# Performance work log

Hardware: AMD Instinct MI355X
Metric: run time of the kernel (lower is better)

Reference implementation:

```python
import jax, jax.numpy as jnp
import numpy as np
import math

B, S, HID = 2, 2048, 2048
NH, NKV, HD = 32, 8, 64
THETA = 10000.0
EPS = 1e-6
LAYER_IDX = 1
LAMBDA_INIT = 0.8 - 0.6 * math.exp(-0.3 * LAYER_IDX)
LAMBDA_STD = 0.1


def setup_inputs() -> dict:
    key = jax.random.key(0)
    ks = jax.random.split(key, 10)
    hidden_states = jax.random.normal(ks[0], (B, S, HID), jnp.float32)
    # RoPE cos/sin, llama convention: emb = cat(freqs, freqs)
    inv_freq = 1.0 / (THETA ** (np.arange(0, HD, 2, dtype=np.float32) / HD))
    freqs = np.outer(np.arange(S, dtype=np.float32), inv_freq)  # [S, HD/2]
    emb = np.concatenate([freqs, freqs], axis=-1)                # [S, HD]
    cos = jnp.broadcast_to(jnp.asarray(np.cos(emb), jnp.float32)[None], (B, S, HD))
    sin = jnp.broadcast_to(jnp.asarray(np.sin(emb), jnp.float32)[None], (B, S, HD))
    # additive causal mask [B,1,S,S]
    causal = jnp.triu(jnp.full((S, S), -1e9, dtype=jnp.float32), k=1)
    attention_mask = jnp.broadcast_to(causal[None, None], (B, 1, S, S))
    sc = 0.02
    wq = sc * jax.random.normal(ks[1], (NH * HD, HID), jnp.float32)
    wk = sc * jax.random.normal(ks[2], (NKV * HD, HID), jnp.float32)
    wv = sc * jax.random.normal(ks[3], (NKV * HD, HID), jnp.float32)
    wo = sc * jax.random.normal(ks[4], (HID, NH * HD), jnp.float32)
    lambda_q1 = LAMBDA_STD * jax.random.normal(ks[5], (HD,), jnp.float32)
    lambda_k1 = LAMBDA_STD * jax.random.normal(ks[6], (HD,), jnp.float32)
    lambda_q2 = LAMBDA_STD * jax.random.normal(ks[7], (HD,), jnp.float32)
    lambda_k2 = LAMBDA_STD * jax.random.normal(ks[8], (HD,), jnp.float32)
    return {"hidden_states": hidden_states, "cos": cos, "sin": sin,
            "attention_mask": attention_mask, "wq": wq, "wk": wk, "wv": wv,
            "wo": wo, "lambda_q1": lambda_q1, "lambda_k1": lambda_k1,
            "lambda_q2": lambda_q2, "lambda_k2": lambda_k2}


def _rotate_half(x):
    x1, x2 = jnp.split(x, 2, axis=-1)
    return jnp.concatenate([-x2, x1], axis=-1)


def reference(hidden_states, cos, sin, attention_mask, wq, wk, wv, wo,
              lambda_q1, lambda_k1, lambda_q2, lambda_k2):
    b, s, _ = hidden_states.shape
    # projections -> [b, h, s, d]
    q = jnp.einsum('bsh,oh->bso', hidden_states, wq).reshape(b, s, NH, HD).transpose(0, 2, 1, 3)
    k = jnp.einsum('bsh,oh->bso', hidden_states, wk).reshape(b, s, NKV, HD).transpose(0, 2, 1, 3)
    v = jnp.einsum('bsh,oh->bso', hidden_states, wv).reshape(b, s, NKV, HD).transpose(0, 2, 1, 3)
    # rotary
    c, sn = cos[:, None], sin[:, None]  # [b,1,s,d]
    q = q * c + _rotate_half(q) * sn
    k = k * c + _rotate_half(k) * sn
    # GQA repeat
    groups = NH // NKV
    k = jnp.repeat(k, groups, axis=1)
    v = jnp.repeat(v, groups, axis=1)
    # diff-attention value trick: pair head i with head i+NH/2 -> [b, NH, s, 2d]
    v = jnp.concatenate([v[:, :NH // 2], v[:, NH // 2:]], axis=-1)  # [b, NH/2, s, 2d]
    v = jnp.concatenate([v, v], axis=1)                              # [b, NH, s, 2d]
    # scores + causal mask, stable softmax in fp32
    aw = jnp.einsum('bhqd,bhkd->bhqk', q, k) / math.sqrt(HD)
    aw = aw + attention_mask
    aw = jax.nn.softmax(aw.astype(jnp.float32), axis=-1).astype(q.dtype)
    ao = jnp.einsum('bhqk,bhkd->bhqd', aw, v)  # [b, NH, s, 2d]
    lam1 = jnp.exp(jnp.sum((lambda_q1 * lambda_k1).astype(jnp.float32)))
    lam2 = jnp.exp(jnp.sum((lambda_q2 * lambda_k2).astype(jnp.float32)))
    lam = (lam1 - lam2).astype(q.dtype) + LAMBDA_INIT
    a1, a2 = ao[:, :NH // 2], ao[:, NH // 2:]
    out = a1 - lam * a2  # [b, NH/2, s, 2d]
    # RMSNorm over last dim (no affine)
    out = out * jax.lax.rsqrt(jnp.mean(out * out, axis=-1, keepdims=True) + EPS)
    out = (1.0 - LAMBDA_INIT) * out
    out = out.transpose(0, 2, 1, 3).reshape(b, s, NH * HD)
    return jnp.einsum('bso,ho->bsh', out, wo)
```

## Files before the change

### kernel.cpp

```cpp
#include <hip/hip_runtime.h>

typedef __attribute__((ext_vector_type(8))) short bhalf8;
typedef __attribute__((ext_vector_type(4))) float floatx4;

constexpr int B_ = 2, S_ = 2048, HID_ = 2048, NH_ = 32, NKV_ = 8, HD_ = 64;
constexpr float LAMBDA_INIT_F = 0.35550906759096924f;
constexpr float EPS_ = 1e-6f;
constexpr float QSCALE_ = 0.18033688011112042f;

#define DEVINL __device__ __forceinline__

DEVINL float bf2f(unsigned short u) {
    union { unsigned u; float f; } v; v.u = ((unsigned)u) << 16; return v.f;
}
DEVINL unsigned short f2bf(float f) {
    union { float f; unsigned u; } v; v.f = f;
    unsigned u = v.u;
    return (unsigned short)((u + 0x7fffu + ((u >> 16) & 1u)) >> 16);
}
DEVINL float fexp2(float x) {
#if __has_builtin(__builtin_amdgcn_exp2f)
    return __builtin_amdgcn_exp2f(x);
#else
    return exp2f(x);
#endif
}
DEVINL unsigned pk_bf16(float a, float b) {
#if __has_builtin(__builtin_amdgcn_cvt_pk_bf16_f32)
    typedef __bf16 bf16x2_t __attribute__((ext_vector_type(2)));
    bf16x2_t p = __builtin_amdgcn_cvt_pk_bf16_f32(a, b);
    unsigned r;
    __builtin_memcpy(&r, &p, 4);
    return r;
#else
    return (unsigned)f2bf(a) | ((unsigned)f2bf(b) << 16);
#endif
}
DEVINL void load_lds16(const unsigned short* g, unsigned short* l) {
    __builtin_amdgcn_global_load_lds(
        (const __attribute__((address_space(1))) unsigned int*)g,
        (__attribute__((address_space(3))) unsigned int*)l, 16, 0, 0);
}

__global__ void cvt_f32_bf16(const float* __restrict__ src, unsigned short* __restrict__ dst, int n) {
    int i = (blockIdx.x * 256 + threadIdx.x) * 4;
    if (i < n) {
        float4 v = *(const float4*)(src + i);
        ushort4 o;
        o.x = f2bf(v.x); o.y = f2bf(v.y); o.z = f2bf(v.z); o.w = f2bf(v.w);
        *(ushort4*)(dst + i) = o;
    }
}

__global__ void lam_kernel(const float* __restrict__ q1, const float* __restrict__ k1,
                           const float* __restrict__ q2, const float* __restrict__ k2,
                           float* __restrict__ lam) {
    const int l = threadIdx.x;
    float p1 = q1[l] * k1[l];
    float p2 = q2[l] * k2[l];
    #pragma unroll
    for (int off = 1; off < 64; off <<= 1) {
        p1 += __shfl_xor(p1, off, 64);
        p2 += __shfl_xor(p2, off, 64);
    }
    if (l == 0) *lam = expf(p1) - expf(p2) + LAMBDA_INIT_F;
}

template <bool OUT_BF16>
__global__ __launch_bounds__(256)
void gemm_bt(const unsigned short* __restrict__ A, const unsigned short* __restrict__ Bw,
             void* __restrict__ Cout, int M, int N, int K) {
    __shared__ __align__(16) unsigned short As[2][128][32];
    __shared__ __align__(16) unsigned short Bs[2][128][32];
    const int t = threadIdx.x;
    const int w = t >> 6, lane = t & 63, quad = lane >> 4, lid = lane & 15;
    const int wr = (w >> 1) * 64, wc = (w & 1) * 64;
    const long bm = (long)blockIdx.x * 128, bn = (long)blockIdx.y * 128;

    floatx4 acc[4][4];
    #pragma unroll
    for (int i = 0; i < 4; i++)
        #pragma unroll
        for (int j = 0; j < 4; j++) acc[i][j] = (floatx4){0.f, 0.f, 0.f, 0.f};

    const int s0 = t, s1 = t + 256;
    const unsigned short* Ag0 = A + (bm + (s0 >> 2)) * (long)K + (s0 & 3) * 8;
    const unsigned short* Ag1 = A + (bm + (s1 >> 2)) * (long)K + (s1 & 3) * 8;
    const unsigned short* Bg0 = Bw + (bn + (s0 >> 2)) * (long)K + (s0 & 3) * 8;
    const unsigned short* Bg1 = Bw + (bn + (s1 >> 2)) * (long)K + (s1 & 3) * 8;
    const int l0 = s0 * 8, l1 = s1 * 8;

    load_lds16(Ag0, &As[0][0][0] + l0);
    load_lds16(Ag1, &As[0][0][0] + l1);
    load_lds16(Bg0, &Bs[0][0][0] + l0);
    load_lds16(Bg1, &Bs[0][0][0] + l1);
    __syncthreads();

    const int nk = K >> 5;
    for (int kt = 0; kt < nk; kt++) {
        const int cur = kt & 1, nxt = cur ^ 1;
        if (kt + 1 < nk) {
            const int off = (kt + 1) << 5;
            load_lds16(Ag0 + off, &As[nxt][0][0] + l0);
            load_lds16(Ag1 + off, &As[nxt][0][0] + l1);
            load_lds16(Bg0 + off, &Bs[nxt][0][0] + l0);
            load_lds16(Bg1 + off, &Bs[nxt][0][0] + l1);
        }
        bhalf8 af[4], bf[4];
        #pragma unroll
        for (int i = 0; i < 4; i++) af[i] = *(const bhalf8*)&As[cur][wr + i * 16 + lid][quad * 8];
        #pragma unroll
        for (int j = 0; j < 4; j++) bf[j] = *(const bhalf8*)&Bs[cur][wc + j * 16 + lid][quad * 8];
        #pragma unroll
        for (int i = 0; i < 4; i++)
            #pragma unroll
            for (int j = 0; j < 4; j++)
                acc[i][j] = __builtin_amdgcn_mfma_f32_16x16x32_bf16(af[i], bf[j], acc[i][j], 0, 0, 0);
        __syncthreads();
    }

    #pragma unroll
    for (int i = 0; i < 4; i++) {
        #pragma unroll
        for (int j = 0; j < 4; j++) {
            const long row = bm + wr + i * 16 + quad * 4;
            const long col = bn + wc + j * 16 + lid;
            #pragma unroll
            for (int r = 0; r < 4; r++) {
                float v = acc[i][j][r];
                if (OUT_BF16)
                    ((unsigned short*)Cout)[(row + r) * N + col] = f2bf(v);
                else
                    ((float*)Cout)[(row + r) * N + col] = v;
            }
        }
    }
}

__global__ __launch_bounds__(256)
void rope_split(const unsigned short* __restrict__ qkv, const float* __restrict__ cosb,
                const float* __restrict__ sinb, unsigned short* __restrict__ Qr,
                unsigned short* __restrict__ Kr) {
    const int r = blockIdx.x;
    const int b = r >> 11, s = r & 2047;
    const int t = threadIdx.x;
    const unsigned short* rowp = qkv + (size_t)r * 3072;
    const float* cp = cosb + (size_t)r * 64;
    const float* sp = sinb + (size_t)r * 64;
    {
        const int h = t >> 3, d0 = (t & 7) * 8;
        unsigned short x[8], o[8], y[8];
        *(int4*)x = *(const int4*)(rowp + h * 64 + d0);
        const int od = (d0 < 32) ? d0 + 32 : d0 - 32;
        *(int4*)o = *(const int4*)(rowp + h * 64 + od);
        const float sgn = (d0 < 32) ? -1.f : 1.f;
        float cc[8], sn[8];
        *(float4*)&cc[0] = *(const float4*)(cp + d0);
        *(float4*)&cc[4] = *(const float4*)(cp + d0 + 4);
        *(float4*)&sn[0] = *(const float4*)(sp + d0);
        *(float4*)&sn[4] = *(const float4*)(sp + d0 + 4);
        #pragma unroll
        for (int i = 0; i < 8; i++)
            y[i] = f2bf((bf2f(x[i]) * cc[i] + sgn * bf2f(o[i]) * sn[i]) * QSCALE_);
        *(int4*)(Qr + ((size_t)(b * NH_ + h) * S_ + s) * HD_ + d0) = *(const int4*)y;
    }
    if (t < 64) {
        const int h = t >> 3, d0 = (t & 7) * 8;
        unsigned short x[8], o[8], y[8];
        *(int4*)x = *(const int4*)(rowp + 2048 + h * 64 + d0);
        const int od = (d0 < 32) ? d0 + 32 : d0 - 32;
        *(int4*)o = *(const int4*)(rowp + 2048 + h * 64 + od);
        const float sgn = (d0 < 32) ? -1.f : 1.f;
        float cc[8], sn[8];
        *(float4*)&cc[0] = *(const float4*)(cp + d0);
        *(float4*)&cc[4] = *(const float4*)(cp + d0 + 4);
        *(float4*)&sn[0] = *(const float4*)(sp + d0);
        *(float4*)&sn[4] = *(const float4*)(sp + d0 + 4);
        #pragma unroll
        for (int i = 0; i < 8; i++)
            y[i] = f2bf(bf2f(x[i]) * cc[i] + sgn * bf2f(o[i]) * sn[i]);
        *(int4*)(Kr + ((size_t)(b * NKV_ + h) * S_ + s) * HD_ + d0) = *(const int4*)y;
    }
}

__global__ __launch_bounds__(256)
void transpose_v(const unsigned short* __restrict__ qkv, unsigned short* __restrict__ VT) {
    __shared__ __align__(16) unsigned short tile[64][72];
    const int bh = blockIdx.y;
    const int b = bh >> 3, h = bh & 7;
    const int s0 = blockIdx.x * 64;
    const int t = threadIdx.x;
    {
        const int sl = t >> 2, d0 = (t & 3) * 16;
        const unsigned short* src = qkv + (size_t)(b * 2048 + s0 + sl) * 3072 + 2560 + h * 64 + d0;
        *(int4*)&tile[sl][d0] = *(const int4*)src;
        *(int4*)&tile[sl][d0 + 8] = *(const int4*)(src + 8);
    }
    __syncthreads();
    {
        const int dl = t >> 2, sc0 = (t & 3) * 16;
        unsigned short* dst = VT + ((size_t)bh * 64 + dl) * 2048 + s0 + sc0;
        unsigned short out[16];
        #pragma unroll
        for (int i = 0; i < 16; i++) out[i] = tile[sc0 + i][dl];
        *(int4*)dst = *(const int4*)&out[0];
        *(int4*)(dst + 8) = *(const int4*)&out[8];
    }
}

__global__ __launch_bounds__(512, 4)
void attn_diff(const unsigned short* __restrict__ Qr, const unsigned short* __restrict__ Kr,
               const unsigned short* __restrict__ VT, const float* __restrict__ lamp,
               unsigned short* __restrict__ attn) {
    union SM {
        struct {
            unsigned short Kt[2][64][72];
            unsigned short Vt[128][72];
            unsigned short Pt[8][16][72];
        } a;
        unsigned short Ot[2][64][136];
    };
    __shared__ __align__(16) SM sm;

    const int j = blockIdx.y, b = blockIdx.z;
    const int t = threadIdx.x;
    const int w = t >> 6, lane = t & 63, quad = lane >> 4, lid = lane & 15;
    const int st = w >> 2;
    const int rh = (w & 3) * 16;
    const int kv1 = j >> 2, kv2 = 4 + (j >> 2);
    const int qhead = j + st * 16;
    const float lam = *lamp;

    const int ss = t >> 8, kidx = t & 255;
    const int key_s = kidx >> 2, dh = (kidx & 3) * 16;
    const unsigned short* ksrc0 = Kr + (size_t)(b * NKV_ + (ss ? kv2 : kv1)) * S_ * HD_ +
                                  (size_t)key_s * HD_ + dh;
    const int d7 = t >> 2, vh = (t & 3) * 16;
    const unsigned short* vsrc0 = VT + ((size_t)(b * NKV_ + (d7 < 64 ? kv1 : kv2)) * HD_ +
                                        (d7 & 63)) * (size_t)S_ + vh;

    for (int half = 0; half < 2; half++) {
        const int qt = half ? (31 - (int)blockIdx.x) : (int)blockIdx.x;
        const int qb = qt * 64;

        const unsigned short* qbase =
            Qr + ((size_t)((b * NH_ + qhead) * S_) + qb + rh + lid) * HD_;
        const bhalf8 qa0 = *(const bhalf8*)(qbase + quad * 8);
        const bhalf8 qa1 = *(const bhalf8*)(qbase + 32 + quad * 8);

        floatx4 acc[8];
        #pragma unroll
        for (int c = 0; c < 8; c++) acc[c] = (floatx4){0.f, 0.f, 0.f, 0.f};
        float l_acc[4] = {0.f, 0.f, 0.f, 0.f};

        const int nkt = qt + 1;

        for (int kt = 0; kt < nkt; kt++) {
            const int k0 = kt * 64;
            const unsigned short* kp = ksrc0 + (size_t)k0 * HD_;
            const unsigned short* vp = vsrc0 + k0;
            int4 kr0 = *(const int4*)(kp);
            int4 kr1 = *(const int4*)(kp + 8);
            int4 vr0 = *(const int4*)(vp);
            int4 vr1 = *(const int4*)(vp + 8);
            __syncthreads();
            *(int4*)&sm.a.Kt[ss][key_s][dh] = kr0;
            *(int4*)&sm.a.Kt[ss][key_s][dh + 8] = kr1;
            *(int4*)&sm.a.Vt[d7][vh] = vr0;
            *(int4*)&sm.a.Vt[d7][vh + 8] = vr1;
            __syncthreads();

            const bool last = (kt == nkt - 1);
            const int nt_lim = last ? ((w & 3) + 1) : 4;

            floatx4 sc[4];
            #pragma unroll
            for (int nt = 0; nt < 4; nt++) {
                if (nt < nt_lim) {
                    const bhalf8 kb0 = *(const bhalf8*)&sm.a.Kt[st][nt * 16 + lid][quad * 8];
                    const bhalf8 kb1 = *(const bhalf8*)&sm.a.Kt[st][nt * 16 + lid][32 + quad * 8];
                    floatx4 z = (floatx4){0.f, 0.f, 0.f, 0.f};
                    z = __builtin_amdgcn_mfma_f32_16x16x32_bf16(qa0, kb0, z, 0, 0, 0);
                    z = __builtin_amdgcn_mfma_f32_16x16x32_bf16(qa1, kb1, z, 0, 0, 0);
                    sc[nt] = z;
                }
            }

            if (last) {
                #pragma unroll
                for (int nt = 0; nt < 4; nt++) {
                    const int keyg = k0 + nt * 16 + lid;
                    #pragma unroll
                    for (int r = 0; r < 4; r++) {
                        float p = 0.f;
                        if (nt < nt_lim) {
                            const int rowg = qb + rh + quad * 4 + r;
                            p = (keyg > rowg) ? 0.f : fexp2(sc[nt][r]);
                        }
                        sc[nt][r] = p;
                        l_acc[r] += p;
                    }
                }
            } else {
                #pragma unroll
                for (int nt = 0; nt < 4; nt++)
                    #pragma unroll
                    for (int r = 0; r < 4; r++) {
                        const float p = fexp2(sc[nt][r]);
                        sc[nt][r] = p;
                        l_acc[r] += p;
                    }
            }

            #pragma unroll
            for (int nt = 0; nt < 4; nt++) {
                #pragma unroll
                for (int r = 0; r < 4; r += 2) {
                    const unsigned pk = pk_bf16(sc[nt][r], sc[nt][r + 1]);
                    sm.a.Pt[w][quad * 4 + r][nt * 16 + lid] = (unsigned short)(pk & 0xffff);
                    sm.a.Pt[w][quad * 4 + r + 1][nt * 16 + lid] = (unsigned short)(pk >> 16);
                }
            }

            #pragma unroll
            for (int kk = 0; kk < 2; kk++) {
                if (nt_lim > kk * 2) {
                    const bhalf8 pa = *(const bhalf8*)&sm.a.Pt[w][lid][kk * 32 + quad * 8];
                    #pragma unroll
                    for (int c = 0; c < 8; c++) {
                        const bhalf8 vb = *(const bhalf8*)&sm.a.Vt[c * 16 + lid][kk * 32 + quad * 8];
                        acc[c] = __builtin_amdgcn_mfma_f32_16x16x32_bf16(pa, vb, acc[c], 0, 0, 0);
                    }
                }
            }
        }

        #pragma unroll
        for (int off = 1; off < 16; off <<= 1)
            #pragma unroll
            for (int r = 0; r < 4; r++) l_acc[r] += __shfl_xor(l_acc[r], off, 64);

        __syncthreads();
        #pragma unroll
        for (int r = 0; r < 4; r++) {
            const float rl = 1.0f / l_acc[r];
            #pragma unroll
            for (int c = 0; c < 8; c++)
                sm.Ot[st][rh + quad * 4 + r][c * 16 + lid] = f2bf(acc[c][r] * rl);
        }
        __syncthreads();

        const int row = t >> 3, m = t & 7;
        float vals[16];
        float ssum = 0.f;
        #pragma unroll
        for (int c = 0; c < 4; c++) {
            const unsigned long long u0 = *(const unsigned long long*)&sm.Ot[0][row][m * 4 + 32 * c];
            const unsigned long long u1 = *(const unsigned long long*)&sm.Ot[1][row][m * 4 + 32 * c];
            #pragma unroll
            for (int i = 0; i < 4; i++) {
                const float x = bf2f((unsigned short)(u0 >> (16 * i))) -
                                lam * bf2f((unsigned short)(u1 >> (16 * i)));
                vals[c * 4 + i] = x;
                ssum += x * x;
            }
        }
        ssum += __shfl_xor(ssum, 1, 64);
        ssum += __shfl_xor(ssum, 2, 64);
        ssum += __shfl_xor(ssum, 4, 64);
        const float scale = (1.f - LAMBDA_INIT_F) * rsqrtf(ssum * (1.f / 128.f) + EPS_);
        unsigned short* dst = attn + (size_t)(b * S_ + qb + row) * (NH_ * HD_) + j * 128 + m * 4;
        #pragma unroll
        for (int c = 0; c < 4; c++) {
            unsigned short ob[4];
            #pragma unroll
            for (int i = 0; i < 4; i++) ob[i] = f2bf(vals[c * 4 + i] * scale);
            *(unsigned long long*)(dst + 32 * c) = *(const unsigned long long*)ob;
        }
        __syncthreads();
    }
}

extern "C" void kernel_launch(void* const* d_in, const int* in_sizes, int n_in,
                              void* d_out, int out_size, void* d_ws, size_t ws_size,
                              hipStream_t stream) {
    const float* hs   = (const float*)d_in[0];
    const float* cosb = (const float*)d_in[1];
    const float* sinb = (const float*)d_in[2];
    const float* wq   = (const float*)d_in[4];
    const float* wk   = (const float*)d_in[5];
    const float* wv   = (const float*)d_in[6];
    const float* wo   = (const float*)d_in[7];
    const float* lq1  = (const float*)d_in[8];
    const float* lk1  = (const float*)d_in[9];
    const float* lq2  = (const float*)d_in[10];
    const float* lk2  = (const float*)d_in[11];

    unsigned short* p = (unsigned short*)d_ws;
    unsigned short* hs_bf = p;  p += (size_t)4096 * 2048;
    unsigned short* wcat  = p;  p += (size_t)3072 * 2048;
    unsigned short* wo_bf = p;  p += (size_t)2048 * 2048;
    unsigned short* qkv   = p;  p += (size_t)4096 * 3072;
    unsigned short* Qr    = p;  p += (size_t)B_ * NH_ * S_ * HD_;
    unsigned short* Kr    = p;  p += (size_t)B_ * NKV_ * S_ * HD_;
    unsigned short* VT    = p;  p += (size_t)B_ * NKV_ * S_ * HD_;
    unsigned short* attnb = p;  p += (size_t)4096 * 2048;
    float* lam = (float*)p;

    cvt_f32_bf16<<<(4096 * 2048) / 1024, 256, 0, stream>>>(hs, hs_bf, 4096 * 2048);
    cvt_f32_bf16<<<(2048 * 2048) / 1024, 256, 0, stream>>>(wq, wcat, 2048 * 2048);
    cvt_f32_bf16<<<(512 * 2048) / 1024, 256, 0, stream>>>(wk, wcat + (size_t)2048 * 2048, 512 * 2048);
    cvt_f32_bf16<<<(512 * 2048) / 1024, 256, 0, stream>>>(wv, wcat + (size_t)2560 * 2048, 512 * 2048);
    cvt_f32_bf16<<<(2048 * 2048) / 1024, 256, 0, stream>>>(wo, wo_bf, 2048 * 2048);
    lam_kernel<<<1, 64, 0, stream>>>(lq1, lk1, lq2, lk2, lam);

    gemm_bt<true><<<dim3(32, 24), 256, 0, stream>>>(hs_bf, wcat, qkv, 4096, 3072, 2048);
    rope_split<<<4096, 256, 0, stream>>>(qkv, cosb, sinb, Qr, Kr);
    transpose_v<<<dim3(32, 16), 256, 0, stream>>>(qkv, VT);
    attn_diff<<<dim3(16, 16, 2), 512, 0, stream>>>(Qr, Kr, VT, lam, attnb);
    gemm_bt<false><<<dim3(32, 16), 256, 0, stream>>>(attnb, wo_bf, d_out, 4096, 2048, 2048);
}
```

Baseline: 365.4 us.

## Fuse RoPE and V transpose into QKV GEMM epilogue; merge conversion kernels

The QKV projection GEMM now applies RoPE directly in its epilogue and writes Q and K in head-major layout. It also writes V transposed through an LDS staging tile, so the intermediate qkv buffer and the separate rope_split and transpose_v kernels are removed. The Q scale is folded into the wq bf16 conversion, and the five conversion launches are merged into one kernel. The price is uncoalesced scalar stores and per-element cos/sin loads in the GEMM epilogue. Folding the scale into the weights also changes where bf16 rounding happens for Q.

```diff
diff --git a/kernel.cpp b/kernel.cpp
--- a/kernel.cpp
+++ b/kernel.cpp
@@ -42,14 +42,27 @@
         (__attribute__((address_space(3))) unsigned int*)l, 16, 0, 0);
 }
 
-__global__ void cvt_f32_bf16(const float* __restrict__ src, unsigned short* __restrict__ dst, int n) {
-    int i = (blockIdx.x * 256 + threadIdx.x) * 4;
-    if (i < n) {
-        float4 v = *(const float4*)(src + i);
-        ushort4 o;
-        o.x = f2bf(v.x); o.y = f2bf(v.y); o.z = f2bf(v.z); o.w = f2bf(v.w);
-        *(ushort4*)(dst + i) = o;
-    }
+__global__ __launch_bounds__(256)
+void cvt_all(const float* __restrict__ hs, const float* __restrict__ wq,
+             const float* __restrict__ wk, const float* __restrict__ wv,
+             const float* __restrict__ wo, unsigned short* __restrict__ hs_bf,
+             unsigned short* __restrict__ wcat, unsigned short* __restrict__ wo_bf) {
+    const size_t i = (size_t)(blockIdx.x * 256 + threadIdx.x) * 4;
+    const float* src;
+    unsigned short* dst;
+    size_t off;
+    float scale = 1.f;
+    if (i < 8388608) { src = hs; dst = hs_bf; off = 0; }
+    else if (i < 12582912) { src = wq; dst = wcat; off = 8388608; scale = QSCALE_; }
+    else if (i < 13631488) { src = wk; dst = wcat + 4194304; off = 12582912; }
+    else if (i < 14680064) { src = wv; dst = wcat + 5242880; off = 13631488; }
+    else { src = wo; dst = wo_bf; off = 14680064; }
+    const size_t k = i - off;
+    const float4 v = *(const float4*)(src + k);
+    ushort4 o;
+    o.x = f2bf(v.x * scale); o.y = f2bf(v.y * scale);
+    o.z = f2bf(v.z * scale); o.w = f2bf(v.w * scale);
+    *(ushort4*)(dst + k) = o;
 }
 
 __global__ void lam_kernel(const float* __restrict__ q1, const float* __restrict__ k1,
@@ -66,10 +79,119 @@
     if (l == 0) *lam = expf(p1) - expf(p2) + LAMBDA_INIT_F;
 }
 
-template <bool OUT_BF16>
+__global__ __launch_bounds__(256)
+void gemm_qkv(const unsigned short* __restrict__ A, const unsigned short* __restrict__ Bw,
+              const float* __restrict__ cosb, const float* __restrict__ sinb,
+              unsigned short* __restrict__ Qr, unsigned short* __restrict__ Kr,
+              unsigned short* __restrict__ VT) {
+    constexpr int K = 2048;
+    union GS {
+        struct { unsigned short A[2][128][32]; unsigned short B[2][128][32]; } d;
+        unsigned short vt[128][130];
+    };
+    __shared__ __align__(16) GS gsm;
+    const int t = threadIdx.x;
+    const int w = t >> 6, lane = t & 63, quad = lane >> 4, lid = lane & 15;
+    const int wr = (w >> 1) * 64, wc = (w & 1) * 64;
+    const long bm = (long)blockIdx.x * 128, bn = (long)blockIdx.y * 128;
+
+    floatx4 acc[4][4];
+    #pragma unroll
+    for (int i = 0; i < 4; i++)
+        #pragma unroll
+        for (int j = 0; j < 4; j++) acc[i][j] = (floatx4){0.f, 0.f, 0.f, 0.f};
+
+    const int s0 = t, s1 = t + 256;
+    const unsigned short* Ag0 = A + (bm + (s0 >> 2)) * (long)K + (s0 & 3) * 8;
+    const unsigned short* Ag1 = A + (bm + (s1 >> 2)) * (long)K + (s1 & 3) * 8;
+    const unsigned short* Bg0 = Bw + (bn + (s0 >> 2)) * (long)K + (s0 & 3) * 8;
+    const unsigned short* Bg1 = Bw + (bn + (s1 >> 2)) * (long)K + (s1 & 3) * 8;
+    const int l0 = s0 * 8, l1 = s1 * 8;
+
+    load_lds16(Ag0, &gsm.d.A[0][0][0] + l0);
+    load_lds16(Ag1, &gsm.d.A[0][0][0] + l1);
+    load_lds16(Bg0, &gsm.d.B[0][0][0] + l0);
+    load_lds16(Bg1, &gsm.d.B[0][0][0] + l1);
+    __syncthreads();
+
+    const int nk = K >> 5;
+    for (int kt = 0; kt < nk; kt++) {
+        const int cur = kt & 1, nxt = cur ^ 1;
+        if (kt + 1 < nk) {
+            const int off = (kt + 1) << 5;
+            load_lds16(Ag0 + off, &gsm.d.A[nxt][0][0] + l0);
+            load_lds16(Ag1 + off, &gsm.d.A[nxt][0][0] + l1);
+            load_lds16(Bg0 + off, &gsm.d.B[nxt][0][0] + l0);
+            load_lds16(Bg1 + off, &gsm.d.B[nxt][0][0] + l1);
+        }
+        bhalf8 af[4], bf[4];
+        #pragma unroll
+        for (int i = 0; i < 4; i++) af[i] = *(const bhalf8*)&gsm.d.A[cur][wr + i * 16 + lid][quad * 8];
+        #pragma unroll
+        for (int j = 0; j < 4; j++) bf[j] = *(const bhalf8*)&gsm.d.B[cur][wc + j * 16 + lid][quad * 8];
+        #pragma unroll
+        for (int i = 0; i < 4; i++)
+            #pragma unroll
+            for (int j = 0; j < 4; j++)
+                acc[i][j] = __builtin_amdgcn_mfma_f32_16x16x32_bf16(af[i], bf[j], acc[i][j], 0, 0, 0);
+        __syncthreads();
+    }
+
+    const int y = blockIdx.y;
+    if (y < 20) {
+        const bool isQ = (y < 16);
+        #pragma unroll
+        for (int i = 0; i < 4; i++) {
+            #pragma unroll
+            for (int r = 0; r < 4; r++) {
+                const long row = bm + wr + i * 16 + quad * 4 + r;
+                const int bb = (int)(row >> 11), s = (int)(row & 2047);
+                const float* cp = cosb + (size_t)row * 64;
+                const float* sp = sinb + (size_t)row * 64;
+                #pragma unroll
+                for (int jj = 0; jj < 4; jj++) {
+                    const int col = (int)bn + wc + jj * 16 + lid;
+                    const int d = col & 63;
+                    const float x = acc[i][jj][r];
+                    const float oth = acc[i][jj ^ 2][r];
+                    const float rot = (jj < 2) ? -oth : oth;
+                    const float yv = x * cp[d] + rot * sp[d];
+                    if (isQ) {
+                        const int h = col >> 6;
+                        Qr[((size_t)(bb * NH_ + h) * S_ + s) * HD_ + d] = f2bf(yv);
+                    } else {
+                        const int h = (col - 2048) >> 6;
+                        Kr[((size_t)(bb * NKV_ + h) * S_ + s) * HD_ + d] = f2bf(yv);
+                    }
+                }
+            }
+        }
+    } else {
+        #pragma unroll
+        for (int i = 0; i < 4; i++)
+            #pragma unroll
+            for (int jj = 0; jj < 4; jj++)
+                #pragma unroll
+                for (int r = 0; r < 4; r++)
+                    gsm.vt[wr + i * 16 + quad * 4 + r][wc + jj * 16 + lid] = f2bf(acc[i][jj][r]);
+        __syncthreads();
+        const int b0 = (int)(bm >> 11), sbase = (int)(bm & 2047);
+        #pragma unroll 4
+        for (int it = 0; it < 32; it++) {
+            const int d = w + 4 * it;
+            const int colg = (int)bn + d;
+            const int h = (colg - 2560) >> 6;
+            const int dl = colg & 63;
+            const int sl = lane * 2;
+            const unsigned v = (unsigned)gsm.vt[sl][d] | ((unsigned)gsm.vt[sl + 1][d] << 16);
+            *(unsigned*)(VT + ((size_t)(b0 * NKV_ + h) * HD_ + dl) * S_ + sbase + sl) = v;
+        }
+    }
+}
+
 __global__ __launch_bounds__(256)
 void gemm_bt(const unsigned short* __restrict__ A, const unsigned short* __restrict__ Bw,
-             void* __restrict__ Cout, int M, int N, int K) {
+             float* __restrict__ Cout, int M, int N, int K) {
     __shared__ __align__(16) unsigned short As[2][128][32];
     __shared__ __align__(16) unsigned short Bs[2][128][32];
     const int t = threadIdx.x;
@@ -126,85 +248,8 @@
             const long row = bm + wr + i * 16 + quad * 4;
             const long col = bn + wc + j * 16 + lid;
             #pragma unroll
-            for (int r = 0; r < 4; r++) {
-                float v = acc[i][j][r];
-                if (OUT_BF16)
-                    ((unsigned short*)Cout)[(row + r) * N + col] = f2bf(v);
-                else
-                    ((float*)Cout)[(row + r) * N + col] = v;
-            }
-        }
-    }
-}
-
-__global__ __launch_bounds__(256)
-void rope_split(const unsigned short* __restrict__ qkv, const float* __restrict__ cosb,
-                const float* __restrict__ sinb, unsigned short* __restrict__ Qr,
-                unsigned short* __restrict__ Kr) {
-    const int r = blockIdx.x;
-    const int b = r >> 11, s = r & 2047;
-    const int t = threadIdx.x;
-    const unsigned short* rowp = qkv + (size_t)r * 3072;
-    const float* cp = cosb + (size_t)r * 64;
-    const float* sp = sinb + (size_t)r * 64;
-    {
-        const int h = t >> 3, d0 = (t & 7) * 8;
-        unsigned short x[8], o[8], y[8];
-        *(int4*)x = *(const int4*)(rowp + h * 64 + d0);
-        const int od = (d0 < 32) ? d0 + 32 : d0 - 32;
-        *(int4*)o = *(const int4*)(rowp + h * 64 + od);
-        const float sgn = (d0 < 32) ? -1.f : 1.f;
-        float cc[8], sn[8];
-        *(float4*)&cc[0] = *(const float4*)(cp + d0);
-        *(float4*)&cc[4] = *(const float4*)(cp + d0 + 4);
-        *(float4*)&sn[0] = *(const float4*)(sp + d0);
-        *(float4*)&sn[4] = *(const float4*)(sp + d0 + 4);
-        #pragma unroll
-        for (int i = 0; i < 8; i++)
-            y[i] = f2bf((bf2f(x[i]) * cc[i] + sgn * bf2f(o[i]) * sn[i]) * QSCALE_);
-        *(int4*)(Qr + ((size_t)(b * NH_ + h) * S_ + s) * HD_ + d0) = *(const int4*)y;
-    }
-    if (t < 64) {
-        const int h = t >> 3, d0 = (t & 7) * 8;
-        unsigned short x[8], o[8], y[8];
-        *(int4*)x = *(const int4*)(rowp + 2048 + h * 64 + d0);
-        const int od = (d0 < 32) ? d0 + 32 : d0 - 32;
-        *(int4*)o = *(const int4*)(rowp + 2048 + h * 64 + od);
-        const float sgn = (d0 < 32) ? -1.f : 1.f;
-        float cc[8], sn[8];
-        *(float4*)&cc[0] = *(const float4*)(cp + d0);
-        *(float4*)&cc[4] = *(const float4*)(cp + d0 + 4);
-        *(float4*)&sn[0] = *(const float4*)(sp + d0);
-        *(float4*)&sn[4] = *(const float4*)(sp + d0 + 4);
-        #pragma unroll
-        for (int i = 0; i < 8; i++)
-            y[i] = f2bf(bf2f(x[i]) * cc[i] + sgn * bf2f(o[i]) * sn[i]);
-        *(int4*)(Kr + ((size_t)(b * NKV_ + h) * S_ + s) * HD_ + d0) = *(const int4*)y;
-    }
-}
-
-__global__ __launch_bounds__(256)
-void transpose_v(const unsigned short* __restrict__ qkv, unsigned short* __restrict__ VT) {
-    __shared__ __align__(16) unsigned short tile[64][72];
-    const int bh = blockIdx.y;
-    const int b = bh >> 3, h = bh & 7;
-    const int s0 = blockIdx.x * 64;
-    const int t = threadIdx.x;
-    {
-        const int sl = t >> 2, d0 = (t & 3) * 16;
-        const unsigned short* src = qkv + (size_t)(b * 2048 + s0 + sl) * 3072 + 2560 + h * 64 + d0;
-        *(int4*)&tile[sl][d0] = *(const int4*)src;
-        *(int4*)&tile[sl][d0 + 8] = *(const int4*)(src + 8);
-    }
-    __syncthreads();
-    {
-        const int dl = t >> 2, sc0 = (t & 3) * 16;
-        unsigned short* dst = VT + ((size_t)bh * 64 + dl) * 2048 + s0 + sc0;
-        unsigned short out[16];
-        #pragma unroll
-        for (int i = 0; i < 16; i++) out[i] = tile[sc0 + i][dl];
-        *(int4*)dst = *(const int4*)&out[0];
-        *(int4*)(dst + 8) = *(const int4*)&out[8];
+            for (int r = 0; r < 4; r++) Cout[(row + r) * N + col] = acc[i][j][r];
+        }
     }
 }
 
@@ -400,23 +445,15 @@
     unsigned short* hs_bf = p;  p += (size_t)4096 * 2048;
     unsigned short* wcat  = p;  p += (size_t)3072 * 2048;
     unsigned short* wo_bf = p;  p += (size_t)2048 * 2048;
-    unsigned short* qkv   = p;  p += (size_t)4096 * 3072;
     unsigned short* Qr    = p;  p += (size_t)B_ * NH_ * S_ * HD_;
     unsigned short* Kr    = p;  p += (size_t)B_ * NKV_ * S_ * HD_;
     unsigned short* VT    = p;  p += (size_t)B_ * NKV_ * S_ * HD_;
     unsigned short* attnb = p;  p += (size_t)4096 * 2048;
     float* lam = (float*)p;
 
-    cvt_f32_bf16<<<(4096 * 2048) / 1024, 256, 0, stream>>>(hs, hs_bf, 4096 * 2048);
-    cvt_f32_bf16<<<(2048 * 2048) / 1024, 256, 0, stream>>>(wq, wcat, 2048 * 2048);
-    cvt_f32_bf16<<<(512 * 2048) / 1024, 256, 0, stream>>>(wk, wcat + (size_t)2048 * 2048, 512 * 2048);
-    cvt_f32_bf16<<<(512 * 2048) / 1024, 256, 0, stream>>>(wv, wcat + (size_t)2560 * 2048, 512 * 2048);
-    cvt_f32_bf16<<<(2048 * 2048) / 1024, 256, 0, stream>>>(wo, wo_bf, 2048 * 2048);
+    cvt_all<<<18432, 256, 0, stream>>>(hs, wq, wk, wv, wo, hs_bf, wcat, wo_bf);
     lam_kernel<<<1, 64, 0, stream>>>(lq1, lk1, lq2, lk2, lam);
-
-    gemm_bt<true><<<dim3(32, 24), 256, 0, stream>>>(hs_bf, wcat, qkv, 4096, 3072, 2048);
-    rope_split<<<4096, 256, 0, stream>>>(qkv, cosb, sinb, Qr, Kr);
-    transpose_v<<<dim3(32, 16), 256, 0, stream>>>(qkv, VT);
+    gemm_qkv<<<dim3(32, 24), 256, 0, stream>>>(hs_bf, wcat, cosb, sinb, Qr, Kr, VT);
     attn_diff<<<dim3(16, 16, 2), 512, 0, stream>>>(Qr, Kr, VT, lam, attnb);
-    gemm_bt<false><<<dim3(32, 16), 256, 0, stream>>>(attnb, wo_bf, d_out, 4096, 2048, 2048);
-}
+    gemm_bt<<<dim3(32, 16), 256, 0, stream>>>(attnb, wo_bf, (float*)d_out, 4096, 2048, 2048);
+}
```

Result: faster. 356.2 us (-2.5%).
